# Kernel tuning notes

Measured on AMD Instinct MI355X. Metric: run time of the kernel, lower is better.

The kernel has to match this reference:

```python
import jax, jax.numpy as jnp
import numpy as np

NEG = -1e30  # log-space 'zero' (avoid real -inf for stable exp/grad)


def _ctc_loss_mean(logp, targets, target_lengths, blank):
    """CTC loss, PyTorch semantics (reduction='mean', zero_infinity=True).
    logp: (B, T, V) log-probabilities; targets: (B, L) padded labels;
    target_lengths: (B,) ints. All input lengths are T (uniform here).
    """
    B, T, V = logp.shape
    L = targets.shape[1]
    S = 2 * L + 1  # extended label length: blank-interleaved

    ext = jnp.full((B, S), blank, dtype=targets.dtype)
    ext = ext.at[:, 1::2].set(targets)  # blanks at even s, labels at odd s

    s = jnp.arange(S)
    valid = s[None, :] < (2 * target_lengths + 1)[:, None]  # (B, S)
    prev2 = jnp.pad(ext[:, :-2], ((0, 0), (2, 0)), constant_values=blank)
    # skip transition s-2 -> s allowed only at non-blank s with no label repeat
    allow_skip = (s[None, :] >= 2) & (ext != blank) & (ext != prev2)

    # per-(t, s) emission log-prob, masked outside valid extended labels
    emit = jnp.take_along_axis(
        logp, jnp.broadcast_to(ext[:, None, :], (B, T, S)), axis=2
    )  # (B, T, S)
    emit = jnp.where(valid[:, None, :], emit, NEG)

    alpha0 = jnp.full((B, S), NEG, dtype=logp.dtype)
    alpha0 = alpha0.at[:, 0].set(emit[:, 0, 0])
    alpha0 = alpha0.at[:, 1].set(emit[:, 0, 1])

    def step(alpha, e):
        a1 = alpha
        a2 = jnp.pad(alpha[:, :-1], ((0, 0), (1, 0)), constant_values=NEG)
        a3 = jnp.pad(alpha[:, :-2], ((0, 0), (2, 0)), constant_values=NEG)
        a3 = jnp.where(allow_skip, a3, NEG)
        m = jnp.maximum(jnp.maximum(a1, a2), a3)
        new = m + jnp.log(jnp.exp(a1 - m) + jnp.exp(a2 - m) + jnp.exp(a3 - m)) + e
        return new, None

    alpha, _ = jax.lax.scan(step, alpha0, jnp.swapaxes(emit, 0, 1)[1:])

    i1 = (2 * target_lengths).astype(jnp.int32)
    l1 = jnp.take_along_axis(alpha, i1[:, None], axis=1)[:, 0]
    l2 = jnp.take_along_axis(alpha, jnp.maximum(i1 - 1, 0)[:, None], axis=1)[:, 0]
    l2 = jnp.where(target_lengths > 0, l2, NEG)
    m = jnp.maximum(l1, l2)
    loss = -(m + jnp.log(jnp.exp(l1 - m) + jnp.exp(l2 - m)))  # (B,)
    loss = jnp.where(loss > 1e20, 0.0, loss)  # zero_infinity=True
    # reduction='mean': divide by target length, then batch mean
    return jnp.mean(loss / jnp.maximum(target_lengths, 1).astype(loss.dtype))


def setup_inputs() -> dict:
    key = jax.random.key(0)
    kl, kt, kn = jax.random.split(key, 3)
    B, T, V, L = 32, 1024, 1000, 256
    logits = jax.random.normal(kl, (B, T, V), dtype=jnp.float32)
    targets = jax.random.randint(kt, (B, L), 1, V).astype(jnp.int32)
    lengths = jax.random.randint(kn, (B,), L // 2 + 2, L + 1)
    target_padding_mask = jnp.arange(L)[None, :] < lengths[:, None]  # bool (B, L)
    return {"logits": logits, "targets": targets,
            "target_padding_mask": target_padding_mask}


def reference(logits, targets, target_padding_mask):
    blank = 0
    lg = logits[:, :-1, :]            # drop last frame
    tgt = targets[:, 1:]              # drop leading (SOS) token
    logp = jax.nn.log_softmax(lg, axis=-1)  # (B, T-1, V)
    tlen = target_padding_mask.sum(axis=1).astype(jnp.int32) - 1
    return _ctc_loss_mean(logp, tgt, tlen, blank)
```

## Files before the change

kernel.cpp:

```cpp
#include <hip/hip_runtime.h>

#define LOG2E 1.4426950408889634f
#define LN2   0.6931471805599453

static constexpr int B  = 32;
static constexpr int T  = 1024;
static constexpr int TT = 1023;
static constexpr int V  = 1000;
static constexpr int L  = 256;
static constexpr int S  = 511;
static constexpr int SP = 512;
static constexpr int TP = 1024;

using h8  = __attribute__((ext_vector_type(8))) _Float16;
using f4  = __attribute__((ext_vector_type(4))) float;
using i4  = __attribute__((ext_vector_type(4))) int;

__device__ __forceinline__ float fexp2(float x) {
#if __has_builtin(__builtin_amdgcn_exp2f)
  return __builtin_amdgcn_exp2f(x);
#else
  return exp2f(x);
#endif
}
__device__ __forceinline__ float flog2(float x) {
#if __has_builtin(__builtin_amdgcn_logf)
  return __builtin_amdgcn_logf(x);
#else
  return log2f(x);
#endif
}

#if __has_builtin(__builtin_amdgcn_update_dpp)
__device__ __forceinline__ float shr1f(float x) {
  int r = __builtin_amdgcn_update_dpp(0, __float_as_int(x), 0x138, 0xf, 0xf, true);
  return __int_as_float(r);
}
__device__ __forceinline__ int shl1i(int x) {
  return __builtin_amdgcn_update_dpp(0, x, 0x130, 0xf, 0xf, true);
}
#define DPP_SWITCH(T, OLD, SRC, BC)                                            \
  T r;                                                                         \
  switch (ctrl) {                                                              \
    case 0x111: r = __builtin_amdgcn_update_dpp(OLD, SRC, 0x111, 0xf, 0xf, BC); break; \
    case 0x112: r = __builtin_amdgcn_update_dpp(OLD, SRC, 0x112, 0xf, 0xf, BC); break; \
    case 0x114: r = __builtin_amdgcn_update_dpp(OLD, SRC, 0x114, 0xf, 0xf, BC); break; \
    case 0x118: r = __builtin_amdgcn_update_dpp(OLD, SRC, 0x118, 0xf, 0xf, BC); break; \
    case 0x142: r = __builtin_amdgcn_update_dpp(OLD, SRC, 0x142, 0xf, 0xf, BC); break; \
    default:    r = __builtin_amdgcn_update_dpp(OLD, SRC, 0x143, 0xf, 0xf, BC); break; \
  }

__device__ __forceinline__ int dppmax_step(int m, const int ctrl) {
  DPP_SWITCH(int, 0, m, true);
  return max(m, r);
}
__device__ __forceinline__ int wavemax_to_sgpr(int m) {
  m = dppmax_step(m, 0x111);
  m = dppmax_step(m, 0x112);
  m = dppmax_step(m, 0x114);
  m = dppmax_step(m, 0x118);
  m = dppmax_step(m, 0x142);
  m = dppmax_step(m, 0x143);
  return __builtin_amdgcn_readlane(m, 63);
}
__device__ __forceinline__ float dppfmax_step(float x, const int ctrl) {
  int xi = __float_as_int(x);
  DPP_SWITCH(int, xi, xi, false);
  return fmaxf(x, __int_as_float(r));
}
__device__ __forceinline__ float wavefmax(float x) {
  x = dppfmax_step(x, 0x111);
  x = dppfmax_step(x, 0x112);
  x = dppfmax_step(x, 0x114);
  x = dppfmax_step(x, 0x118);
  x = dppfmax_step(x, 0x142);
  x = dppfmax_step(x, 0x143);
  return __int_as_float(__builtin_amdgcn_readlane(__float_as_int(x), 63));
}
__device__ __forceinline__ float dppfadd_step(float x, const int ctrl) {
  DPP_SWITCH(int, 0, __float_as_int(x), true);
  return x + __int_as_float(r);
}
__device__ __forceinline__ float wavefsum(float x) {
  x = dppfadd_step(x, 0x111);
  x = dppfadd_step(x, 0x112);
  x = dppfadd_step(x, 0x114);
  x = dppfadd_step(x, 0x118);
  x = dppfadd_step(x, 0x142);
  x = dppfadd_step(x, 0x143);
  return __int_as_float(__builtin_amdgcn_readlane(__float_as_int(x), 63));
}
#else
__device__ __forceinline__ float shr1f(float x) {
  float r = __shfl_up(x, 1, 64);
  return (threadIdx.x & 63) == 0 ? 0.0f : r;
}
__device__ __forceinline__ int shl1i(int x) {
  int r = __shfl_down(x, 1, 64);
  return (threadIdx.x & 63) == 63 ? 0 : r;
}
__device__ __forceinline__ int wavemax_to_sgpr(int m) {
  for (int o = 32; o >= 1; o >>= 1) m = max(m, __shfl_xor(m, o, 64));
  return m;
}
__device__ __forceinline__ float wavefmax(float x) {
  for (int o = 32; o >= 1; o >>= 1) x = fmaxf(x, __shfl_xor(x, o, 64));
  return x;
}
__device__ __forceinline__ float wavefsum(float x) {
  for (int o = 32; o >= 1; o >>= 1) x += __shfl_xor(x, o, 64);
  return x;
}
#endif

__global__ void k_tlen(const unsigned char* __restrict__ maskb,
                       int* __restrict__ tlen) {
  int b = blockIdx.x;
  int lane = threadIdx.x;
  int ca = 0;
  for (int k = lane; k < L; k += 64) ca += (maskb[b * L + k] != 0) ? 1 : 0;
  for (int o = 32; o >= 1; o >>= 1) ca += __shfl_xor(ca, o, 64);
  int cnt = ca;
  if (ca < 130) {
    const int* mi = (const int*)maskb;
    int cb = 0;
    for (int k = lane; k < L; k += 64) cb += (mi[b * L + k] != 0) ? 1 : 0;
    for (int o = 32; o >= 1; o >>= 1) cb += __shfl_xor(cb, o, 64);
    cnt = cb;
  }
  if (lane == 0) tlen[b] = cnt - 1;
}

__global__ __launch_bounds__(256, 4) void k_emit(const float* __restrict__ logits,
                                                 const int* __restrict__ targets,
                                                 const int* __restrict__ tlenp,
                                                 _Float16* __restrict__ E,
                                                 float* __restrict__ G) {
  __shared__ float yrow[4][1024];
  const int wid = threadIdx.x >> 6;
  const int lane = threadIdx.x & 63;
  float* yw = yrow[wid];
  const int w0 = blockIdx.x * 4 + wid;
  const int sb = lane << 3;

#define EISSUE(P, r)                                              \
  do {                                                            \
    int b_ = (r) / TT;                                            \
    int t_ = (r) - b_ * TT;                                       \
    const float* rp_ = logits + ((size_t)b_ * T + t_) * V + (lane << 2); \
    const int* tp_ = targets + b_ * L + (lane << 2);              \
    const int* lp_ = tlenp + b_;                                  \
    asm volatile(                                                 \
      "global_load_dwordx4 %0, %6, off\n\t"                       \
      "global_load_dwordx4 %1, %6, off offset:1024\n\t"           \
      "global_load_dwordx4 %2, %6, off offset:2048\n\t"           \
      "global_load_dwordx4 %3, %6, off offset:3072\n\t"           \
      "global_load_dwordx4 %4, %7, off\n\t"                       \
      "global_load_dword %5, %8, off"                             \
      : "=&v"(P##u0), "=&v"(P##u1), "=&v"(P##u2), "=&v"(P##u3),   \
        "=&v"(P##tv), "=&v"(P##tl)                                \
      : "v"(rp_), "v"(tp_), "v"(lp_));                            \
  } while (0)

#define EWAIT(n, P)                                               \
  do {                                                            \
    asm volatile("s_waitcnt vmcnt(" #n ")"                        \
                 : "+v"(P##u0), "+v"(P##u1), "+v"(P##u2),         \
                   "+v"(P##u3), "+v"(P##tv), "+v"(P##tl));        \
    __builtin_amdgcn_sched_barrier(0);                            \
  } while (0)

#define EPROC(P, r)                                               \
  do {                                                            \
    int b_ = (r) / TT;                                            \
    int t_ = (r) - b_ * TT;                                       \
    f4 v0 = P##u0 * LOG2E;                                        \
    f4 v1 = P##u1 * LOG2E;                                        \
    f4 v2 = P##u2 * LOG2E;                                        \
    f4 v3 = P##u3 * LOG2E;                                        \
    const bool has3 = (lane < 58);         \
    if (!has3) { v3[0] = v3[1] = v3[2] = v3[3] = -2.0e30f; }      \
    reinterpret_cast<f4*>(yw)[lane]       = v0;                   \
    reinterpret_cast<f4*>(yw)[lane + 64]  = v1;                   \
    reinterpret_cast<f4*>(yw)[lane + 128] = v2;                   \
    if (has3) reinterpret_cast<f4*>(yw)[lane + 192] = v3;         \
    float lm = fmaxf(fmaxf(fmaxf(v0[0], v0[1]), fmaxf(v0[2], v0[3])), \
                     fmaxf(fmaxf(v1[0], v1[1]), fmaxf(v1[2], v1[3]))); \
    lm = fmaxf(lm, fmaxf(fmaxf(v2[0], v2[1]), fmaxf(v2[2], v2[3]))); \
    lm = fmaxf(lm, fmaxf(fmaxf(v3[0], v3[1]), fmaxf(v3[2], v3[3]))); \
    const float my = wavefmax(lm);                                \
    float ps = fexp2(v0[0]-my) + fexp2(v0[1]-my) + fexp2(v0[2]-my) + fexp2(v0[3]-my) \
             + fexp2(v1[0]-my) + fexp2(v1[1]-my) + fexp2(v1[2]-my) + fexp2(v1[3]-my) \
             + fexp2(v2[0]-my) + fexp2(v2[1]-my) + fexp2(v2[2]-my) + fexp2(v2[3]-my) \
             + fexp2(v3[0]-my) + fexp2(v3[1]-my) + fexp2(v3[2]-my) + fexp2(v3[3]-my); \
    const float g = -flog2(wavefsum(ps));                         \
    const int smax = 2 * P##tl + 1;                               \
    const int l1 = P##tv[1], l2 = P##tv[2], l3 = P##tv[3];        \
    const int l4 = shl1i(P##tv[0]);              \
    const float eb = fexp2(yw[0]  - my);                          \
    const float e1 = fexp2(yw[l1] - my);                          \
    const float e2 = fexp2(yw[l2] - my);                          \
    const float e3 = fexp2(yw[l3] - my);                          \
    const float e4 = fexp2(yw[l4] - my);                          \
    h8 o;                                                         \
    o[0] = (_Float16)((sb     < smax) ? eb : 0.0f);               \
    o[1] = (_Float16)((sb + 1 < smax) ? e1 : 0.0f);               \
    o[2] = (_Float16)((sb + 2 < smax) ? eb : 0.0f);               \
    o[3] = (_Float16)((sb + 3 < smax) ? e2 : 0.0f);               \
    o[4] = (_Float16)((sb + 4 < smax) ? eb : 0.0f);               \
    o[5] = (_Float16)((sb + 5 < smax) ? e3 : 0.0f);               \
    o[6] = (_Float16)((sb + 6 < smax) ? eb : 0.0f);               \
    o[7] = (_Float16)((lane < 63 && sb + 7 < smax) ? e4 : 0.0f);  \
    reinterpret_cast<h8*>(E + ((size_t)b_ * TP + t_) * SP)[lane] = o; \
    if (lane == 0) G[r] = g;                                      \
  } while (0)

  f4 Au0, Au1, Au2, Au3; i4 Atv; int Atl;
  f4 Bu0, Bu1, Bu2, Bu3; i4 Btv; int Btl;
  f4 Cu0, Cu1, Cu2, Cu3; i4 Ctv; int Ctl;

  EISSUE(A, w0);
  EISSUE(B, w0 + 8184);
  EISSUE(C, w0 + 16368);
  EWAIT(12, A); EPROC(A, w0);
  EISSUE(A, w0 + 24552);
  EWAIT(12, B); EPROC(B, w0 + 8184);
  EWAIT(6,  C); EPROC(C, w0 + 16368);
  EWAIT(0,  A); EPROC(A, w0 + 24552);
#undef EISSUE
#undef EWAIT
#undef EPROC
}

__global__ __launch_bounds__(64, 1) void k_ctc(const _Float16* __restrict__ E,
                                               const int* __restrict__ targets,
                                               const int* __restrict__ tlenp,
                                               const float* __restrict__ G,
                                               float* __restrict__ lossb) {
  const int b = blockIdx.x;
  const int lane = threadIdx.x;
  const int s0 = lane << 3;
  const int* tg = targets + b * L;

  const int tl = tlenp[b];

  double gs = 0.0;
  for (int k = lane; k < TT; k += 64) gs += (double)G[b * TT + k];
  for (int o = 32; o >= 1; o >>= 1) gs += __shfl_xor(gs, o, 64);

  float f1 = 0.0f, f3, f5, f7 = 0.0f;
  {
    int s = s0 + 1;
    if (s >= 3) f1 = (tg[(s + 1) >> 1] != tg[(s - 1) >> 1]) ? 1.0f : 0.0f;
    s = s0 + 3;
    f3 = (tg[(s + 1) >> 1] != tg[(s - 1) >> 1]) ? 1.0f : 0.0f;
    s = s0 + 5;
    f5 = (tg[(s + 1) >> 1] != tg[(s - 1) >> 1]) ? 1.0f : 0.0f;
    s = s0 + 7;
    if (s < S) f7 = (tg[(s + 1) >> 1] != tg[(s - 1) >> 1]) ? 1.0f : 0.0f;
  }

  const _Float16* E0 = E + (size_t)b * TP * SP;
  const _Float16* Ebase = E0 + s0;

  float a0 = (lane == 0) ? (float)E0[0] : 0.0f;
  float a1 = (lane == 0) ? (float)E0[1] : 0.0f;
  float a2 = 0.f, a3 = 0.f, a4 = 0.f, a5 = 0.f, a6 = 0.f, a7 = 0.f;
  float n7 = 0.0f;
  int lsacc = 0;

  asm volatile("" :: "v"(f1), "v"(f3), "v"(f5), "v"(f7),
                     "v"(a0), "v"(a1), "v"(gs), "v"((float)tl));

#define GLROW4(d0, d1, d2, d3, p)                                \
  asm volatile("global_load_dwordx4 %0, %4, off\n\t"             \
               "global_load_dwordx4 %1, %4, off offset:1024\n\t" \
               "global_load_dwordx4 %2, %4, off offset:2048\n\t" \
               "global_load_dwordx4 %3, %4, off offset:3072"     \
               : "=&v"(d0), "=&v"(d1), "=&v"(d2), "=&v"(d3) : "v"(p))

#define LOAD8(P, r0)                                             \
  do {                                                           \
    const _Float16* q_ = Ebase + (size_t)(r0) * SP;              \
    GLROW4(P##0, P##1, P##2, P##3, q_);                          \
    GLROW4(P##4, P##5, P##6, P##7, q_ + 4 * SP);                 \
  } while (0)

#define VMWAIT8(n, P)                                            \
  do {                                                           \
    asm volatile("s_waitcnt vmcnt(" #n ")"                       \
                 : "+v"(P##0), "+v"(P##1), "+v"(P##2), "+v"(P##3), \
                   "+v"(P##4), "+v"(P##5), "+v"(P##6), "+v"(P##7)); \
    __builtin_amdgcn_sched_barrier(0);                           \
  } while (0)

#define MIXLO(D, SSS, HWORD)                                     \
  asm("v_fma_mix_f32 %0, %1, %2, 0 op_sel:[0,0,0] op_sel_hi:[0,1,0]" \
      : "=v"(D) : "v"(SSS), "v"(HWORD))
#define MIXHI(D, SSS, HWORD)                                     \
  asm("v_fma_mix_f32 %0, %1, %2, 0 op_sel:[0,1,0] op_sel_hi:[0,1,0]" \
      : "=v"(D) : "v"(SSS), "v"(HWORD))

#define STEPF(H)                                                \
  do {                                                          \
    i4 hw = __builtin_bit_cast(i4, (H));                        \
    float s7 = fmaf(f7, a5, a6 + a7);                           \
    float t7; MIXHI(t7, s7, hw[3]);                             \
    float n7n = shr1f(t7);                                      \
    float s0 = a0 + n7;                                         \
    float s1 = fmaf(f1, n7, a0 + a1);                           \
    float s2 = a1 + a2;                                         \
    float s3 = fmaf(f3, a1, a2 + a3);                           \
    float s4 = a3 + a4;                                         \
    float s5 = fmaf(f5, a3, a4 + a5);                           \
    float s6 = a5 + a6;                                         \
    float t0, t1, t2, t3, t4, t5, t6;                           \
    MIXLO(t0, s0, hw[0]);                                       \
    MIXHI(t1, s1, hw[0]);                                       \
    MIXLO(t2, s2, hw[1]);                                       \
    MIXHI(t3, s3, hw[1]);                                       \
    MIXLO(t4, s4, hw[2]);                                       \
    MIXHI(t5, s5, hw[2]);                                       \
    MIXLO(t6, s6, hw[3]);                                       \
    a0 = t0; a1 = t1; a2 = t2; a3 = t3;                         \
    a4 = t4; a5 = t5; a6 = t6; a7 = t7;                         \
    n7 = n7n;                                                   \
  } while (0)

#define RESCALE()                                               \
  do {                                                          \
    int m = max(max(max(__float_as_int(a0), __float_as_int(a1)),\
                    max(__float_as_int(a2), __float_as_int(a3))),\
                max(max(__float_as_int(a4), __float_as_int(a5)),\
                    max(__float_as_int(a6), __float_as_int(a7))));\
    int mw = wavemax_to_sgpr(m);                                \
    int e = mw >> 23;                                           \
    int sh = 191 - e;                                           \
    lsacc += e - 191;                                           \
    a0 = ldexpf(a0, sh); a1 = ldexpf(a1, sh);                   \
    a2 = ldexpf(a2, sh); a3 = ldexpf(a3, sh);                   \
    a4 = ldexpf(a4, sh); a5 = ldexpf(a5, sh);                   \
    a6 = ldexpf(a6, sh); a7 = ldexpf(a7, sh);                   \
    n7 = ldexpf(n7, sh);                                        \
  } while (0)

#define PROC8(P)                                                \
  do {                                                          \
    STEPF(P##0); STEPF(P##1); STEPF(P##2); STEPF(P##3);         \
    STEPF(P##4); STEPF(P##5); STEPF(P##6); STEPF(P##7);         \
  } while (0)

  h8 A0, A1, A2, A3, A4, A5, A6, A7;
  h8 B0, B1, B2, B3, B4, B5, B6, B7;
  h8 C0, C1, C2, C3, C4, C5, C6, C7;
  h8 D0, D1, D2, D3, D4, D5, D6, D7;

  LOAD8(A, 1);
  LOAD8(B, 9);
  LOAD8(C, 17);
  LOAD8(D, 25);

  int t = 1;
#pragma unroll 1
  for (int it = 0; it < 30; ++it) {
    RESCALE();
    VMWAIT8(24, A); PROC8(A); LOAD8(A, t + 32);
    VMWAIT8(24, B); PROC8(B); LOAD8(B, t + 40);
    VMWAIT8(24, C); PROC8(C); LOAD8(C, t + 48);
    VMWAIT8(24, D); PROC8(D); LOAD8(D, t + 56);
    t += 32;
  }
  RESCALE();
  VMWAIT8(24, A); PROC8(A); LOAD8(A, 993);
  VMWAIT8(24, B); PROC8(B); LOAD8(B, 1001);
  VMWAIT8(24, C); PROC8(C); LOAD8(C, 1009);
  VMWAIT8(24, D); PROC8(D); LOAD8(D, 1017);
  RESCALE();
  VMWAIT8(24, A); PROC8(A);
  VMWAIT8(16, B); PROC8(B);
  VMWAIT8(8,  C); PROC8(C);
  VMWAIT8(0,  D);
  STEPF(D0); STEPF(D1); STEPF(D2);
  STEPF(D3); STEPF(D4); STEPF(D5);
#undef GLROW4
#undef LOAD8
#undef VMWAIT8
#undef MIXLO
#undef MIXHI
#undef STEPF
#undef RESCALE
#undef PROC8

  {
    int i1 = 2 * tl;
    int j1 = (i1 > 0 ? i1 : 1) - 1;
    float va, vb;
    switch (i1 & 7) {
      case 0: va = a0; break; case 1: va = a1; break;
      case 2: va = a2; break; case 3: va = a3; break;
      case 4: va = a4; break; case 5: va = a5; break;
      case 6: va = a6; break; default: va = a7; break;
    }
    switch (j1 & 7) {
      case 0: vb = a0; break; case 1: vb = a1; break;
      case 2: vb = a2; break; case 3: vb = a3; break;
      case 4: vb = a4; break; case 5: vb = a5; break;
      case 6: vb = a6; break; default: vb = a7; break;
    }
    float l1v = __shfl(va, i1 >> 3, 64);
    float l2v = __shfl(vb, j1 >> 3, 64);
    if (lane == 0) {
      float p = l1v + l2v;
      int hi = __float_as_int(p);
      int ep = (hi >> 23) - 127;
      float pm = ldexpf(p, -ep);
      float lm = flog2(pm);
      double loss2 = -((double)lm + (double)ep + (double)lsacc + gs);
      float loss = (float)(loss2 * LN2);
      if (!(loss <= 1e20f)) loss = 0.0f;
      int dv = (tl > 0) ? tl : 1;
      lossb[b] = loss / (float)dv;
    }
  }
}

__global__ void k_mean(const float* __restrict__ lossb, float* __restrict__ out) {
  int lane = threadIdx.x;
  float v = (lane < B) ? lossb[lane] : 0.0f;
  for (int o = 32; o >= 1; o >>= 1) v += __shfl_xor(v, o, 64);
  if (lane == 0) out[0] = v / (float)B;
}

extern "C" void kernel_launch(void* const* d_in, const int* in_sizes, int n_in,
                              void* d_out, int out_size, void* d_ws, size_t ws_size,
                              hipStream_t stream) {
  const float* logits = (const float*)d_in[0];
  const int* targets = (const int*)d_in[1];
  const unsigned char* mask = (const unsigned char*)d_in[2];

  char* ws = (char*)d_ws;
  int* tlen = (int*)ws;
  float* lossb = (float*)(ws + 128);
  float* G = (float*)(ws + 512);
  _Float16* E = (_Float16*)(ws + 512 + 132 * 1024);

  k_tlen<<<B, 64, 0, stream>>>(mask, tlen);
  k_emit<<<(B * TT) / 16, 256, 0, stream>>>(logits, targets, tlen, E, G);
  k_ctc<<<B, 64, 0, stream>>>(E, targets, tlen, G, lossb);
  k_mean<<<1, 64, 0, stream>>>(lossb, (float*)d_out);
}
```

Before: 88.32 us.

## Drop tlen kernel, compute length in CTC kernel, simplify emit to one row per wave

Removes the separate target-length kernel and computes the length inside the CTC recursion kernel, so emit no longer depends on it. The emit kernel now processes one row per wave with plain loads instead of a hand-pipelined four-row asm scheme, launching four times as many blocks. It folds LOG2E into an fma, packs fp16 output with cvt_pkrtz, and stops masking emissions by length. Invalid states are instead excluded in the CTC kernel's rescale max through per-lane masks. The aim is to save a launch and emit ALU work, at the risk of losing the explicit memory-latency overlap.

After: 84.41 us. -4.4%, faster.

```diff
diff --git a/kernel.cpp b/kernel.cpp
--- a/kernel.cpp
+++ b/kernel.cpp
@@ -13,6 +13,7 @@
 static constexpr int TP = 1024;
 
 using h8  = __attribute__((ext_vector_type(8))) _Float16;
+using hf2 = __attribute__((ext_vector_type(2))) __fp16;
 using f4  = __attribute__((ext_vector_type(4))) float;
 using i4  = __attribute__((ext_vector_type(4))) int;
 
@@ -113,10 +114,7 @@
 }
 #endif
 
-__global__ void k_tlen(const unsigned char* __restrict__ maskb,
-                       int* __restrict__ tlen) {
-  int b = blockIdx.x;
-  int lane = threadIdx.x;
+__device__ __forceinline__ int mask_tlen(const unsigned char* maskb, int b, int lane) {
   int ca = 0;
   for (int k = lane; k < L; k += 64) ca += (maskb[b * L + k] != 0) ? 1 : 0;
   for (int o = 32; o >= 1; o >>= 1) ca += __shfl_xor(ca, o, 64);
@@ -128,113 +126,84 @@
     for (int o = 32; o >= 1; o >>= 1) cb += __shfl_xor(cb, o, 64);
     cnt = cb;
   }
-  if (lane == 0) tlen[b] = cnt - 1;
-}
-
-__global__ __launch_bounds__(256, 4) void k_emit(const float* __restrict__ logits,
-                                                 const int* __restrict__ targets,
-                                                 const int* __restrict__ tlenp,
-                                                 _Float16* __restrict__ E,
-                                                 float* __restrict__ G) {
+  return cnt - 1;
+}
+
+__global__ __launch_bounds__(256) void k_emit(const float* __restrict__ logits,
+                                              const int* __restrict__ targets,
+                                              _Float16* __restrict__ E,
+                                              float* __restrict__ G) {
   __shared__ float yrow[4][1024];
   const int wid = threadIdx.x >> 6;
   const int lane = threadIdx.x & 63;
   float* yw = yrow[wid];
-  const int w0 = blockIdx.x * 4 + wid;
-  const int sb = lane << 3;
-
-#define EISSUE(P, r)                                              \
-  do {                                                            \
-    int b_ = (r) / TT;                                            \
-    int t_ = (r) - b_ * TT;                                       \
-    const float* rp_ = logits + ((size_t)b_ * T + t_) * V + (lane << 2); \
-    const int* tp_ = targets + b_ * L + (lane << 2);              \
-    const int* lp_ = tlenp + b_;                                  \
-    asm volatile(                                                 \
-      "global_load_dwordx4 %0, %6, off\n\t"                       \
-      "global_load_dwordx4 %1, %6, off offset:1024\n\t"           \
-      "global_load_dwordx4 %2, %6, off offset:2048\n\t"           \
-      "global_load_dwordx4 %3, %6, off offset:3072\n\t"           \
-      "global_load_dwordx4 %4, %7, off\n\t"                       \
-      "global_load_dword %5, %8, off"                             \
-      : "=&v"(P##u0), "=&v"(P##u1), "=&v"(P##u2), "=&v"(P##u3),   \
-        "=&v"(P##tv), "=&v"(P##tl)                                \
-      : "v"(rp_), "v"(tp_), "v"(lp_));                            \
-  } while (0)
-
-#define EWAIT(n, P)                                               \
-  do {                                                            \
-    asm volatile("s_waitcnt vmcnt(" #n ")"                        \
-                 : "+v"(P##u0), "+v"(P##u1), "+v"(P##u2),         \
-                   "+v"(P##u3), "+v"(P##tv), "+v"(P##tl));        \
-    __builtin_amdgcn_sched_barrier(0);                            \
-  } while (0)
-
-#define EPROC(P, r)                                               \
-  do {                                                            \
-    int b_ = (r) / TT;                                            \
-    int t_ = (r) - b_ * TT;                                       \
-    f4 v0 = P##u0 * LOG2E;                                        \
-    f4 v1 = P##u1 * LOG2E;                                        \
-    f4 v2 = P##u2 * LOG2E;                                        \
-    f4 v3 = P##u3 * LOG2E;                                        \
-    const bool has3 = (lane < 58);         \
-    if (!has3) { v3[0] = v3[1] = v3[2] = v3[3] = -2.0e30f; }      \
-    reinterpret_cast<f4*>(yw)[lane]       = v0;                   \
-    reinterpret_cast<f4*>(yw)[lane + 64]  = v1;                   \
-    reinterpret_cast<f4*>(yw)[lane + 128] = v2;                   \
-    if (has3) reinterpret_cast<f4*>(yw)[lane + 192] = v3;         \
-    float lm = fmaxf(fmaxf(fmaxf(v0[0], v0[1]), fmaxf(v0[2], v0[3])), \
-                     fmaxf(fmaxf(v1[0], v1[1]), fmaxf(v1[2], v1[3]))); \
-    lm = fmaxf(lm, fmaxf(fmaxf(v2[0], v2[1]), fmaxf(v2[2], v2[3]))); \
-    lm = fmaxf(lm, fmaxf(fmaxf(v3[0], v3[1]), fmaxf(v3[2], v3[3]))); \
-    const float my = wavefmax(lm);                                \
-    float ps = fexp2(v0[0]-my) + fexp2(v0[1]-my) + fexp2(v0[2]-my) + fexp2(v0[3]-my) \
-             + fexp2(v1[0]-my) + fexp2(v1[1]-my) + fexp2(v1[2]-my) + fexp2(v1[3]-my) \
-             + fexp2(v2[0]-my) + fexp2(v2[1]-my) + fexp2(v2[2]-my) + fexp2(v2[3]-my) \
-             + fexp2(v3[0]-my) + fexp2(v3[1]-my) + fexp2(v3[2]-my) + fexp2(v3[3]-my); \
-    const float g = -flog2(wavefsum(ps));                         \
-    const int smax = 2 * P##tl + 1;                               \
-    const int l1 = P##tv[1], l2 = P##tv[2], l3 = P##tv[3];        \
-    const int l4 = shl1i(P##tv[0]);              \
-    const float eb = fexp2(yw[0]  - my);                          \
-    const float e1 = fexp2(yw[l1] - my);                          \
-    const float e2 = fexp2(yw[l2] - my);                          \
-    const float e3 = fexp2(yw[l3] - my);                          \
-    const float e4 = fexp2(yw[l4] - my);                          \
-    h8 o;                                                         \
-    o[0] = (_Float16)((sb     < smax) ? eb : 0.0f);               \
-    o[1] = (_Float16)((sb + 1 < smax) ? e1 : 0.0f);               \
-    o[2] = (_Float16)((sb + 2 < smax) ? eb : 0.0f);               \
-    o[3] = (_Float16)((sb + 3 < smax) ? e2 : 0.0f);               \
-    o[4] = (_Float16)((sb + 4 < smax) ? eb : 0.0f);               \
-    o[5] = (_Float16)((sb + 5 < smax) ? e3 : 0.0f);               \
-    o[6] = (_Float16)((sb + 6 < smax) ? eb : 0.0f);               \
-    o[7] = (_Float16)((lane < 63 && sb + 7 < smax) ? e4 : 0.0f);  \
-    reinterpret_cast<h8*>(E + ((size_t)b_ * TP + t_) * SP)[lane] = o; \
-    if (lane == 0) G[r] = g;                                      \
-  } while (0)
-
-  f4 Au0, Au1, Au2, Au3; i4 Atv; int Atl;
-  f4 Bu0, Bu1, Bu2, Bu3; i4 Btv; int Btl;
-  f4 Cu0, Cu1, Cu2, Cu3; i4 Ctv; int Ctl;
-
-  EISSUE(A, w0);
-  EISSUE(B, w0 + 8184);
-  EISSUE(C, w0 + 16368);
-  EWAIT(12, A); EPROC(A, w0);
-  EISSUE(A, w0 + 24552);
-  EWAIT(12, B); EPROC(B, w0 + 8184);
-  EWAIT(6,  C); EPROC(C, w0 + 16368);
-  EWAIT(0,  A); EPROC(A, w0 + 24552);
-#undef EISSUE
-#undef EWAIT
-#undef EPROC
+  const int r = blockIdx.x * 4 + wid;
+  const int b = r / TT;
+  const int t = r - b * TT;
+
+  const f4* row = reinterpret_cast<const f4*>(logits + ((size_t)b * T + t) * V);
+  f4 u0 = row[lane];
+  f4 u1 = row[lane + 64];
+  f4 u2 = row[lane + 128];
+  const bool has3 = (lane < 58);
+  f4 u3;
+  if (has3) u3 = row[lane + 192];
+  else { u3[0] = u3[1] = u3[2] = u3[3] = -3.0e38f; }
+
+  reinterpret_cast<f4*>(yw)[lane]       = u0;
+  reinterpret_cast<f4*>(yw)[lane + 64]  = u1;
+  reinterpret_cast<f4*>(yw)[lane + 128] = u2;
+  if (has3) reinterpret_cast<f4*>(yw)[lane + 192] = u3;
+
+  float lm = fmaxf(fmaxf(fmaxf(u0[0], u0[1]), fmaxf(u0[2], u0[3])),
+                   fmaxf(fmaxf(u1[0], u1[1]), fmaxf(u1[2], u1[3])));
+  lm = fmaxf(lm, fmaxf(fmaxf(u2[0], u2[1]), fmaxf(u2[2], u2[3])));
+  lm = fmaxf(lm, fmaxf(fmaxf(u3[0], u3[1]), fmaxf(u3[2], u3[3])));
+  const float my = wavefmax(lm);
+  const float c = -my * LOG2E;
+
+  float ps = fexp2(fmaf(u0[0], LOG2E, c)) + fexp2(fmaf(u0[1], LOG2E, c))
+           + fexp2(fmaf(u0[2], LOG2E, c)) + fexp2(fmaf(u0[3], LOG2E, c))
+           + fexp2(fmaf(u1[0], LOG2E, c)) + fexp2(fmaf(u1[1], LOG2E, c))
+           + fexp2(fmaf(u1[2], LOG2E, c)) + fexp2(fmaf(u1[3], LOG2E, c))
+           + fexp2(fmaf(u2[0], LOG2E, c)) + fexp2(fmaf(u2[1], LOG2E, c))
+           + fexp2(fmaf(u2[2], LOG2E, c)) + fexp2(fmaf(u2[3], LOG2E, c))
+           + fexp2(fmaf(u3[0], LOG2E, c)) + fexp2(fmaf(u3[1], LOG2E, c))
+           + fexp2(fmaf(u3[2], LOG2E, c)) + fexp2(fmaf(u3[3], LOG2E, c));
+  const float g = -flog2(wavefsum(ps));
+
+  const int base = b * L + (lane << 2);
+  i4 tv = *reinterpret_cast<const i4*>(targets + base);
+  const int l1 = tv[1], l2 = tv[2], l3 = tv[3];
+  const int l4 = shl1i(tv[0]);
+  const float eb = fexp2(fmaf(yw[0],  LOG2E, c));
+  const float e1 = fexp2(fmaf(yw[l1], LOG2E, c));
+  const float e2 = fexp2(fmaf(yw[l2], LOG2E, c));
+  const float e3 = fexp2(fmaf(yw[l3], LOG2E, c));
+  float e4       = fexp2(fmaf(yw[l4], LOG2E, c));
+  if (lane == 63) e4 = 0.0f;
+
+#if __has_builtin(__builtin_amdgcn_cvt_pkrtz)
+  i4 oi;
+  { hf2 p = __builtin_amdgcn_cvt_pkrtz(eb, e1); oi[0] = __builtin_bit_cast(int, p); }
+  { hf2 p = __builtin_amdgcn_cvt_pkrtz(eb, e2); oi[1] = __builtin_bit_cast(int, p); }
+  { hf2 p = __builtin_amdgcn_cvt_pkrtz(eb, e3); oi[2] = __builtin_bit_cast(int, p); }
+  { hf2 p = __builtin_amdgcn_cvt_pkrtz(eb, e4); oi[3] = __builtin_bit_cast(int, p); }
+  reinterpret_cast<i4*>(E + ((size_t)b * TP + t) * SP)[lane] = oi;
+#else
+  h8 o;
+  o[0] = (_Float16)eb; o[1] = (_Float16)e1;
+  o[2] = (_Float16)eb; o[3] = (_Float16)e2;
+  o[4] = (_Float16)eb; o[5] = (_Float16)e3;
+  o[6] = (_Float16)eb; o[7] = (_Float16)e4;
+  reinterpret_cast<h8*>(E + ((size_t)b * TP + t) * SP)[lane] = o;
+#endif
+  if (lane == 0) G[r] = g;
 }
 
 __global__ __launch_bounds__(64, 1) void k_ctc(const _Float16* __restrict__ E,
                                                const int* __restrict__ targets,
-                                               const int* __restrict__ tlenp,
+                                               const unsigned char* __restrict__ maskb,
                                                const float* __restrict__ G,
                                                float* __restrict__ lossb) {
   const int b = blockIdx.x;
@@ -242,7 +211,7 @@
   const int s0 = lane << 3;
   const int* tg = targets + b * L;
 
-  const int tl = tlenp[b];
+  const int tl = mask_tlen(maskb, b, lane);
 
   double gs = 0.0;
   for (int k = lane; k < TT; k += 64) gs += (double)G[b * TT + k];
@@ -260,6 +229,16 @@
     if (s < S) f7 = (tg[(s + 1) >> 1] != tg[(s - 1) >> 1]) ? 1.0f : 0.0f;
   }
 
+  const int s2t = 2 * tl;
+  const int vm0 = (s0 + 0 <= s2t) ? -1 : 0;
+  const int vm1 = (s0 + 1 <= s2t) ? -1 : 0;
+  const int vm2 = (s0 + 2 <= s2t) ? -1 : 0;
+  const int vm3 = (s0 + 3 <= s2t) ? -1 : 0;
+  const int vm4 = (s0 + 4 <= s2t) ? -1 : 0;
+  const int vm5 = (s0 + 5 <= s2t) ? -1 : 0;
+  const int vm6 = (s0 + 6 <= s2t) ? -1 : 0;
+  const int vm7 = (s0 + 7 <= s2t) ? -1 : 0;
+
   const _Float16* E0 = E + (size_t)b * TP * SP;
   const _Float16* Ebase = E0 + s0;
 
@@ -307,21 +286,21 @@
     float s7 = fmaf(f7, a5, a6 + a7);                           \
     float t7; MIXHI(t7, s7, hw[3]);                             \
     float n7n = shr1f(t7);                                      \
-    float s0 = a0 + n7;                                         \
-    float s1 = fmaf(f1, n7, a0 + a1);                           \
-    float s2 = a1 + a2;                                         \
-    float s3 = fmaf(f3, a1, a2 + a3);                           \
-    float s4 = a3 + a4;                                         \
-    float s5 = fmaf(f5, a3, a4 + a5);                           \
-    float s6 = a5 + a6;                                         \
+    float s0_ = a0 + n7;                                        \
+    float s1_ = fmaf(f1, n7, a0 + a1);                          \
+    float s2_ = a1 + a2;                                        \
+    float s3_ = fmaf(f3, a1, a2 + a3);                          \
+    float s4_ = a3 + a4;                                        \
+    float s5_ = fmaf(f5, a3, a4 + a5);                          \
+    float s6_ = a5 + a6;                                        \
     float t0, t1, t2, t3, t4, t5, t6;                           \
-    MIXLO(t0, s0, hw[0]);                                       \
-    MIXHI(t1, s1, hw[0]);                                       \
-    MIXLO(t2, s2, hw[1]);                                       \
-    MIXHI(t3, s3, hw[1]);                                       \
-    MIXLO(t4, s4, hw[2]);                                       \
-    MIXHI(t5, s5, hw[2]);                                       \
-    MIXLO(t6, s6, hw[3]);                                       \
+    MIXLO(t0, s0_, hw[0]);                                      \
+    MIXHI(t1, s1_, hw[0]);                                      \
+    MIXLO(t2, s2_, hw[1]);                                      \
+    MIXHI(t3, s3_, hw[1]);                                      \
+    MIXLO(t4, s4_, hw[2]);                                      \
+    MIXHI(t5, s5_, hw[2]);                                      \
+    MIXLO(t6, s6_, hw[3]);                                      \
     a0 = t0; a1 = t1; a2 = t2; a3 = t3;                         \
     a4 = t4; a5 = t5; a6 = t6; a7 = t7;                         \
     n7 = n7n;                                                   \
@@ -329,10 +308,14 @@
 
 #define RESCALE()                                               \
   do {                                                          \
-    int m = max(max(max(__float_as_int(a0), __float_as_int(a1)),\
-                    max(__float_as_int(a2), __float_as_int(a3))),\
-                max(max(__float_as_int(a4), __float_as_int(a5)),\
-                    max(__float_as_int(a6), __float_as_int(a7))));\
+    int m = max(max(max(__float_as_int(a0) & vm0,               \
+                        __float_as_int(a1) & vm1),              \
+                    max(__float_as_int(a2) & vm2,               \
+                        __float_as_int(a3) & vm3)),             \
+                max(max(__float_as_int(a4) & vm4,               \
+                        __float_as_int(a5) & vm5),              \
+                    max(__float_as_int(a6) & vm6,               \
+                        __float_as_int(a7) & vm7)));            \
     int mw = wavemax_to_sgpr(m);                                \
     int e = mw >> 23;                                           \
     int sh = 191 - e;                                           \
@@ -439,13 +422,11 @@
   const unsigned char* mask = (const unsigned char*)d_in[2];
 
   char* ws = (char*)d_ws;
-  int* tlen = (int*)ws;
   float* lossb = (float*)(ws + 128);
   float* G = (float*)(ws + 512);
   _Float16* E = (_Float16*)(ws + 512 + 132 * 1024);
 
-  k_tlen<<<B, 64, 0, stream>>>(mask, tlen);
-  k_emit<<<(B * TT) / 16, 256, 0, stream>>>(logits, targets, tlen, E, G);
-  k_ctc<<<B, 64, 0, stream>>>(E, targets, tlen, G, lossb);
+  k_emit<<<(B * TT) / 4, 256, 0, stream>>>(logits, targets, E, G);
+  k_ctc<<<B, 64, 0, stream>>>(E, targets, mask, G, lossb);
   k_mean<<<1, 64, 0, stream>>>(lossb, (float*)d_out);
 }
```
